# Performance work log

Hardware: AMD Instinct MI355X
Metric: run time of the kernel (lower is better)

## Reference

```python
import jax, jax.numpy as jnp
import numpy as np

DIM, NHEADS = 1536, 12
HEAD_DIM = DIM // NHEADS  # 128

def _rope_params(max_pos, d):
    inv = 1.0 / (10000.0 ** (np.arange(0, d, 2, dtype=np.float64) / d))
    ang = np.outer(np.arange(max_pos, dtype=np.float64), inv)
    return np.stack([np.cos(ang), np.sin(ang)], -1).astype(np.float32)  # [max_pos, d//2, 2]

def setup_inputs() -> dict:
    key = jax.random.key(0)
    ks = jax.random.split(key, 8)
    B, F, H, W = 1, 3, 30, 52
    L = F * H * W  # 4680
    def w(k):
        return jax.random.normal(k, (DIM, DIM), jnp.float32) * 0.02
    # Wan rope table: head_dim=128 -> segments of real dim 44, 42, 42 (complex 22,21,21)
    freqs = np.concatenate([_rope_params(1024, 44), _rope_params(1024, 42), _rope_params(1024, 42)], axis=1)
    return {
        "x": jax.random.normal(ks[0], (B, L, DIM), jnp.float32),
        "wq": w(ks[1]), "bq": jnp.zeros((DIM,), jnp.float32),
        "wk": w(ks[2]), "bk": jnp.zeros((DIM,), jnp.float32),
        "wv": w(ks[3]), "bv": jnp.zeros((DIM,), jnp.float32),
        "wo": w(ks[4]), "bo": jnp.zeros((DIM,), jnp.float32),
        "gq": jnp.ones((DIM,), jnp.float32),
        "gk": jnp.ones((DIM,), jnp.float32),
        "freqs": jnp.asarray(freqs),                       # [1024, 64, 2] (cos, sin)
        "seq_lens": jnp.array([L], jnp.int64),
        "grid_sizes": jnp.array([[F, H, W]], jnp.int64),
        "F": F, "H": H, "W": W,
        "sink_size": 1, "local_attn_size": 2,
    }

def _rmsnorm(x, g, eps=1e-6):
    xf = x.astype(jnp.float32)
    return xf * jax.lax.rsqrt(jnp.mean(xf * xf, -1, keepdims=True) + eps) * g

def _rope_table(freqs, F, H, W):
    # freqs: [1024, 64, 2]; split complex dims [22, 21, 21] for (t, h, w)
    c = freqs.shape[1]
    s0 = c - 2 * (c // 3)          # 22
    s1 = c // 3                    # 21
    ft = jnp.broadcast_to(freqs[:F, :s0].reshape(F, 1, 1, s0, 2), (F, H, W, s0, 2))
    fh = jnp.broadcast_to(freqs[:H, s0:s0 + s1].reshape(1, H, 1, s1, 2), (F, H, W, s1, 2))
    fw = jnp.broadcast_to(freqs[:W, s0 + s1:].reshape(1, 1, W, s1, 2), (F, H, W, s1, 2))
    return jnp.concatenate([ft, fh, fw], -2).reshape(F * H * W, c, 2)  # [L, c, 2]

def _apply_rope(t, fr):
    # t: [B, L, n, d]; fr: [L, c, 2] with c = d // 2; complex multiply in real arithmetic
    B, L, n, d = t.shape
    c = d // 2
    tr = t.reshape(B, L, n, c, 2)
    a, b = tr[..., 0], tr[..., 1]
    cos = fr[None, :, None, :, 0]
    sin = fr[None, :, None, :, 1]
    out = jnp.stack([a * cos - b * sin, a * sin + b * cos], -1)
    return out.reshape(B, L, n, d)

def reference(x, wq, bq, wk, bk, wv, bv, wo, bo, gq, gk, freqs, seq_lens, grid_sizes,
              F, H, W, sink_size, local_attn_size):
    B, L, dim = x.shape
    n, d = NHEADS, HEAD_DIM
    q = _rmsnorm(x @ wq.T + bq, gq).reshape(B, L, n, d)
    k = _rmsnorm(x @ wk.T + bk, gk).reshape(B, L, n, d)
    v = (x @ wv.T + bv).reshape(B, L, n, d)
    fr = _rope_table(freqs, F, H, W)
    rq = _apply_rope(q, fr)
    rk = _apply_rope(k, fr)
    # sink + causal local-window block mask at frame granularity
    frame = jnp.arange(L) // (H * W)
    fq, fk = frame[:, None], frame[None, :]
    allow = (fk <= fq) & ((fk < sink_size) | (fq - fk < local_attn_size))  # [L, L]
    scores = jnp.einsum('blnd,bmnd->bnlm', rq, rk) / jnp.sqrt(jnp.float32(d))
    scores = jnp.where(allow[None, None], scores, -jnp.inf)
    p = jax.nn.softmax(scores, axis=-1)
    out = jnp.einsum('bnlm,bmnd->blnd', p, v).reshape(B, L, dim)
    return out @ wo.T + bo
```

## Files before the change

### kernel.cpp

```cpp
#include <hip/hip_runtime.h>

#define L_SEQ 4680
#define DIMSZ 1536
#define NHEAD 12
#define HDIM 128
#define FRAME 1560
#define NKT_ALL 74
#define SCALE_L2E 0.12751743f
#define WSZ 2359296
#define XSZ 7274496
#define PMPITCH 4736

typedef float f32x4 __attribute__((ext_vector_type(4)));
typedef _Float16 f16;
typedef _Float16 f16x2 __attribute__((ext_vector_type(2)));
typedef _Float16 f16x4 __attribute__((ext_vector_type(4)));
typedef _Float16 f16x8 __attribute__((ext_vector_type(8)));
typedef unsigned short u16;

__device__ __forceinline__ void gll16(const void* g, void* l) {
  __builtin_amdgcn_global_load_lds(
      (const __attribute__((address_space(1))) unsigned int*)g,
      (__attribute__((address_space(3))) unsigned int*)l, 16, 0, 0);
}

__global__ __launch_bounds__(256) void split_a16(
    const float* __restrict__ A, int R, f16* __restrict__ out) {
  const int rt = blockIdx.x, kt = blockIdx.y;
  const int t = threadIdx.x;
  const int row = t >> 1, c0 = (t & 1) * 16;
  const int gr = min(rt * 128 + row, R - 1);
  const float* src = &A[(size_t)gr * DIMSZ + kt * 32 + c0];
  float f[16];
#pragma unroll
  for (int i = 0; i < 4; ++i) *(float4*)&f[i * 4] = *(const float4*)&src[i * 4];
  size_t obase = ((size_t)(rt * 48 + kt)) * 4096 + row * 32;
#pragma unroll
  for (int cc = 0; cc < 2; ++cc) {
    f16x8 o;
#pragma unroll
    for (int i = 0; i < 8; ++i) o[i] = (f16)f[cc * 8 + i];
    int s = (c0 >> 3) + cc;
    *(f16x8*)&out[obase + ((s * 8) ^ ((row & 3) * 8))] = o;
  }
}

__global__ __launch_bounds__(256) void split_w16(
    const float* __restrict__ A, f16* __restrict__ hi, f16* __restrict__ lo8) {
  const int rt = blockIdx.x, kt = blockIdx.y;
  const int t = threadIdx.x;
  const int row = t >> 1, c0 = (t & 1) * 16;
  const float* src = &A[(size_t)(rt * 128 + row) * DIMSZ + kt * 32 + c0];
  float f[16];
#pragma unroll
  for (int i = 0; i < 4; ++i) *(float4*)&f[i * 4] = *(const float4*)&src[i * 4];
  size_t obase = ((size_t)(rt * 48 + kt)) * 4096 + row * 32;
#pragma unroll
  for (int cc = 0; cc < 2; ++cc) {
    f16x8 oh, ol;
#pragma unroll
    for (int i = 0; i < 8; ++i) {
      float v = f[cc * 8 + i];
      f16 h = (f16)v;
      oh[i] = h;
      ol[i] = (f16)((v - (float)h) * 256.0f);
    }
    int s = (c0 >> 3) + cc;
    size_t off = obase + ((s * 8) ^ ((row & 3) * 8));
    *(f16x8*)&hi[off] = oh;
    *(f16x8*)&lo8[off] = ol;
  }
}

__global__ __launch_bounds__(256, 3) void gemm_f16(
    const f16* __restrict__ A, const f16* __restrict__ Wh, const f16* __restrict__ Wl,
    const float* __restrict__ b0, const float* __restrict__ b1, const float* __restrict__ b2,
    float* __restrict__ C, int M) {
  __shared__ f16 S[2][3][4096];
  const int t = threadIdx.x;
  const int lane = t & 63, w = t >> 6;
  const int g = lane >> 4, ln = lane & 15;
  const int wm = w >> 1, wn = w & 1;
  const int mt = blockIdx.x, nt = blockIdx.y;
  const int which = nt / 12, ntw = nt - which * 12;
  const float* bias = which == 0 ? b0 : (which == 1 ? b1 : b2);
  const f16* srcs[3] = {A + (size_t)mt * 48 * 4096,
                        Wh + ((size_t)which * 12 + ntw) * 48 * 4096,
                        Wl + ((size_t)which * 12 + ntw) * 48 * 4096};
  float* Cw = C + (size_t)which * ((size_t)L_SEQ * DIMSZ);
  f32x4 acc[4][4] = {};
#pragma unroll
  for (int a = 0; a < 3; ++a)
#pragma unroll
    for (int i = 0; i < 2; ++i)
      gll16(srcs[a] + (i * 256 + t) * 8, &S[0][a][(i * 256 + t) * 8]);
  int buf = 0;
  const f16 sc = (f16)0.00390625f;
  for (int kt = 0; kt < 48; ++kt) {
    __syncthreads();
    if (kt + 1 < 48) {
      int b = buf ^ 1;
#pragma unroll
      for (int a = 0; a < 3; ++a)
#pragma unroll
        for (int i = 0; i < 2; ++i)
          gll16(srcs[a] + (size_t)(kt + 1) * 4096 + (i * 256 + t) * 8,
                &S[b][a][(i * 256 + t) * 8]);
    }
    f16x8 af[4], as[4], wh4[4], wl4[4];
#pragma unroll
    for (int mi = 0; mi < 4; ++mi) {
      int row = wm * 64 + mi * 16 + ln;
      int off = row * 32 + ((g * 8) ^ ((row & 3) * 8));
      af[mi] = *(const f16x8*)&S[buf][0][off];
#pragma unroll
      for (int i = 0; i < 8; ++i) as[mi][i] = af[mi][i] * sc;
    }
#pragma unroll
    for (int ni = 0; ni < 4; ++ni) {
      int row = wn * 64 + ni * 16 + ln;
      int off = row * 32 + ((g * 8) ^ ((row & 3) * 8));
      wh4[ni] = *(const f16x8*)&S[buf][1][off];
      wl4[ni] = *(const f16x8*)&S[buf][2][off];
    }
#pragma unroll
    for (int mi = 0; mi < 4; ++mi)
#pragma unroll
      for (int ni = 0; ni < 4; ++ni) {
        acc[mi][ni] = __builtin_amdgcn_mfma_f32_16x16x32_f16(af[mi], wh4[ni], acc[mi][ni], 0, 0, 0);
        acc[mi][ni] = __builtin_amdgcn_mfma_f32_16x16x32_f16(as[mi], wl4[ni], acc[mi][ni], 0, 0, 0);
      }
    buf ^= 1;
  }
#pragma unroll
  for (int mi = 0; mi < 4; ++mi)
#pragma unroll
    for (int ni = 0; ni < 4; ++ni) {
      int col = ntw * 128 + wn * 64 + ni * 16 + ln;
      float bv = bias[col];
#pragma unroll
      for (int r = 0; r < 4; ++r) {
        int row = mt * 128 + wm * 64 + mi * 16 + 4 * g + r;
        if (row < M) Cw[(size_t)row * DIMSZ + col] = acc[mi][ni][r] + bv;
      }
    }
}

__global__ __launch_bounds__(256) void norm_rope(
    const float* __restrict__ qf, const float* __restrict__ kf,
    const float* __restrict__ gq, const float* __restrict__ gk,
    const float* __restrict__ freqs, f16* __restrict__ q16, f16* __restrict__ k16) {
  const int pos = blockIdx.x;
  const bool isq = blockIdx.y == 0;
  const float* row = (isq ? qf : kf) + (size_t)pos * DIMSZ;
  const float* g = isq ? gq : gk;
  const int t = threadIdx.x;
  float2 ab[3];
  float ss = 0.f;
#pragma unroll
  for (int i = 0; i < 3; ++i) {
    ab[i] = *(const float2*)&row[2 * (t + 256 * i)];
    ss += ab[i].x * ab[i].x + ab[i].y * ab[i].y;
  }
#pragma unroll
  for (int m = 32; m; m >>= 1) ss += __shfl_xor(ss, m);
  __shared__ float part[4];
  if ((t & 63) == 0) part[t >> 6] = ss;
  __syncthreads();
  const float tot = part[0] + part[1] + part[2] + part[3];
  float scale = rsqrtf(tot * (1.f / DIMSZ) + 1e-6f);
  if (isq) scale *= SCALE_L2E;
  const int f = pos / FRAME;
  const int rem = pos - f * FRAME;
  const int hh = rem / 52;
  const int ww = rem - hh * 52;
  const int kt = pos >> 6, kk = pos & 63;
#pragma unroll
  for (int i = 0; i < 3; ++i) {
    const int p = t + 256 * i;
    const int c = p & 63;
    const int h = p >> 6;
    const int pr = c < 22 ? f : (c < 43 ? hh : ww);
    const float cs = freqs[(pr * 64 + c) * 2 + 0];
    const float sn = freqs[(pr * 64 + c) * 2 + 1];
    const float a = ab[i].x * scale * g[2 * p];
    const float b = ab[i].y * scale * g[2 * p + 1];
    f16x2 o;
    o[0] = (f16)(a * cs - b * sn);
    o[1] = (f16)(a * sn + b * cs);
    if (isq) {
      *(f16x2*)&q16[(size_t)pos * DIMSZ + 2 * p] = o;
    } else {
      const int s = c >> 2;
      size_t base = ((size_t)(h * NKT_ALL + kt)) << 13;
      *(f16x2*)&k16[base + kk * 128 + ((s * 8) ^ ((kk & 7) * 8)) + (c & 3) * 2] = o;
    }
  }
}

__global__ __launch_bounds__(256) void vconvert(const float* __restrict__ v, f16* __restrict__ v16) {
  __shared__ f16 Ls[64][136];
  const int kt = blockIdx.x, h = blockIdx.y, t = threadIdx.x;
#pragma unroll
  for (int p = 0; p < 8; ++p) {
    int e = p * 1024 + t * 4;
    int kk = e >> 7, d = e & 127;
    int gr = kt * 64 + kk;
    float4 val = make_float4(0.f, 0.f, 0.f, 0.f);
    if (gr < L_SEQ) val = *(const float4*)&v[(size_t)gr * DIMSZ + h * HDIM + d];
    f16x4 o;
    o[0] = (f16)val.x; o[1] = (f16)val.y; o[2] = (f16)val.z; o[3] = (f16)val.w;
    *(f16x4*)&Ls[kk][d] = o;
  }
  __syncthreads();
  f16* out = v16 + (((size_t)(h * NKT_ALL + kt)) << 13);
#pragma unroll
  for (int p = 0; p < 4; ++p) {
    int idx = p * 256 + t;
    int d = idx >> 3, kg = idx & 7;
    f16x8 o;
#pragma unroll
    for (int i = 0; i < 8; ++i) o[i] = Ls[kg * 8 + i][d];
    *(f16x8*)&out[d * 64 + ((kg * 8) ^ ((d & 7) * 8))] = o;
  }
}

__global__ __launch_bounds__(256, 2) void attn_split(
    const f16* __restrict__ q16, const f16* __restrict__ k16,
    const f16* __restrict__ v16, float* __restrict__ pO,
    float* __restrict__ pm, float* __restrict__ pl) {
  __shared__ f16 Ks[2][8192];
  __shared__ f16 Vt[2][8192];
  __shared__ float Os[4][16][20];
  const int b = blockIdx.x;
  const int qt = 36 - b / 24;
  const int rem = b % 24;
  const int s = rem / 12;
  const int h = rem % 12;
  const int q0 = qt * 128;
  const int t = threadIdx.x;
  const int lane = t & 63, w = t >> 6;
  const int g = lane >> 4, ln = lane & 15;

  f16x8 qa[2][4];
  int klim[2];
  float m_run[2], l_run[2];
#pragma unroll
  for (int mi = 0; mi < 2; ++mi) {
    int qrow = min(q0 + w * 32 + mi * 16 + ln, L_SEQ - 1);
    klim[mi] = (qrow / FRAME + 1) * FRAME;
    m_run[mi] = -1e30f;
    l_run[mi] = 0.f;
    const f16* qb = &q16[(size_t)qrow * DIMSZ + h * HDIM + g * 8];
#pragma unroll
    for (int kc = 0; kc < 4; ++kc) qa[mi][kc] = *(const f16x8*)&qb[kc * 32];
  }
  const int klim0 = __shfl(klim[0], 0);
  f32x4 acc[2][8] = {};

  const int rmax = min(q0 + 127, L_SEQ - 1);
  const int nkt = ((rmax / FRAME + 1) * FRAME + 63) >> 6;
  const size_t hbase = ((size_t)h * NKT_ALL) << 13;
  {
    size_t tb = hbase + ((size_t)s << 13);
#pragma unroll
    for (int i = 0; i < 4; ++i) {
      gll16(k16 + tb + (i * 256 + t) * 8, &Ks[0][(i * 256 + t) * 8]);
      gll16(v16 + tb + (i * 256 + t) * 8, &Vt[0][(i * 256 + t) * 8]);
    }
  }
  int buf = 0;
  for (int kt = s; kt < nkt; kt += 2) {
    __syncthreads();
    if (kt + 2 < nkt) {
      size_t tb = hbase + ((size_t)(kt + 2) << 13);
      int nb_ = buf ^ 1;
#pragma unroll
      for (int i = 0; i < 4; ++i) {
        gll16(k16 + tb + (i * 256 + t) * 8, &Ks[nb_][(i * 256 + t) * 8]);
        gll16(v16 + tb + (i * 256 + t) * 8, &Vt[nb_][(i * 256 + t) * 8]);
      }
    }
    const f16* Kb = Ks[buf];
    const f16* Vb = Vt[buf];

    f32x4 st[2][4] = {};
    __builtin_amdgcn_s_setprio(1);
#pragma unroll
    for (int nb = 0; nb < 4; ++nb) {
      int row = nb * 16 + ln;
      f16x8 kb[4];
#pragma unroll
      for (int kc = 0; kc < 4; ++kc)
        kb[kc] = *(const f16x8*)&Kb[row * 128 + ((g * 8 + kc * 32) ^ ((row & 7) * 8))];
#pragma unroll
      for (int kc = 0; kc < 4; ++kc) {
        st[0][nb] = __builtin_amdgcn_mfma_f32_16x16x32_f16(kb[kc], qa[0][kc], st[0][nb], 0, 0, 0);
        st[1][nb] = __builtin_amdgcn_mfma_f32_16x16x32_f16(kb[kc], qa[1][kc], st[1][nb], 0, 0, 0);
      }
    }
    __builtin_amdgcn_s_setprio(0);

    f16x4 pb[2][4];
    const bool boundary = (kt * 64 + 64 > klim0);
#pragma unroll
    for (int mi = 0; mi < 2; ++mi) {
      float pv4[4][4];
      float rm = -1e30f;
      if (boundary) {
#pragma unroll
        for (int nb = 0; nb < 4; ++nb)
#pragma unroll
          for (int r = 0; r < 4; ++r) {
            int key = kt * 64 + nb * 16 + 4 * g + r;
            float val = st[mi][nb][r];
            if (key >= klim[mi]) val = -1e30f;
            pv4[nb][r] = val;
            rm = fmaxf(rm, val);
          }
      } else {
#pragma unroll
        for (int nb = 0; nb < 4; ++nb)
#pragma unroll
          for (int r = 0; r < 4; ++r) {
            float val = st[mi][nb][r];
            pv4[nb][r] = val;
            rm = fmaxf(rm, val);
          }
      }
      rm = fmaxf(rm, __shfl_xor(rm, 16));
      rm = fmaxf(rm, __shfl_xor(rm, 32));
      if (!__all(rm - m_run[mi] <= 8.0f)) {
        float mn = fmaxf(m_run[mi], rm);
        float fs = exp2f(m_run[mi] - mn);
        m_run[mi] = mn;
        l_run[mi] *= fs;
#pragma unroll
        for (int db = 0; db < 8; ++db)
#pragma unroll
          for (int r = 0; r < 4; ++r) acc[mi][db][r] *= fs;
      }
      float sm = 0.f;
#pragma unroll
      for (int nb = 0; nb < 4; ++nb)
#pragma unroll
        for (int r = 0; r < 4; ++r) {
          float e = exp2f(pv4[nb][r] - m_run[mi]);
          sm += e;
          pb[mi][nb][r] = (f16)e;
        }
      sm += __shfl_xor(sm, 16);
      sm += __shfl_xor(sm, 32);
      l_run[mi] += sm;
    }

    __builtin_amdgcn_s_setprio(1);
#pragma unroll
    for (int db = 0; db < 8; ++db) {
      int d = db * 16 + ln;
#pragma unroll
      for (int nb = 0; nb < 4; ++nb) {
        f16x4 va = *(const f16x4*)&Vb[d * 64 + ((nb * 16 + 4 * g) ^ ((d & 7) * 8))];
        acc[0][db] = __builtin_amdgcn_mfma_f32_16x16x16f16(va, pb[0][nb], acc[0][db], 0, 0, 0);
        acc[1][db] = __builtin_amdgcn_mfma_f32_16x16x16f16(va, pb[1][nb], acc[1][db], 0, 0, 0);
      }
    }
    __builtin_amdgcn_s_setprio(0);
    buf ^= 1;
  }

#pragma unroll
  for (int mi = 0; mi < 2; ++mi) {
    int qrow = q0 + w * 32 + mi * 16 + ln;
    if (g == 0) {
      pm[((size_t)s * 12 + h) * PMPITCH + qrow] = m_run[mi];
      pl[((size_t)s * 12 + h) * PMPITCH + qrow] = l_run[mi];
    }
#pragma unroll
    for (int db = 0; db < 8; ++db) {
      *(f32x4*)&Os[w][ln][4 * g] = acc[mi][db];
      asm volatile("s_waitcnt lgkmcnt(0)" ::: "memory");
#pragma unroll
      for (int r = 0; r < 4; ++r) {
        int q = q0 + w * 32 + mi * 16 + 4 * g + r;
        float val = Os[w][4 * g + r][ln];
        if (q < L_SEQ)
          pO[((size_t)s * L_SEQ + q) * DIMSZ + h * HDIM + db * 16 + ln] = val;
      }
      asm volatile("s_waitcnt lgkmcnt(0)" ::: "memory");
    }
  }
}

__global__ __launch_bounds__(256) void combine_k(
    const float* __restrict__ pO, const float* __restrict__ pm,
    const float* __restrict__ pl, f16* __restrict__ aos) {
  const int qt = blockIdx.x, h = blockIdx.y, t = threadIdx.x;
  const int row = t >> 1, d0 = (t & 1) * 64;
  const int q = min(qt * 128 + row, L_SEQ - 1);
  const float m0 = pm[(size_t)h * PMPITCH + q];
  const float m1 = pm[((size_t)12 + h) * PMPITCH + q];
  const float l0 = pl[(size_t)h * PMPITCH + q];
  const float l1 = pl[((size_t)12 + h) * PMPITCH + q];
  const float m = fmaxf(m0, m1);
  float w0 = exp2f(m0 - m), w1 = exp2f(m1 - m);
  const float rinv = 1.f / (w0 * l0 + w1 * l1);
  w0 *= rinv; w1 *= rinv;
  const float* o0 = &pO[(size_t)q * DIMSZ + h * HDIM + d0];
  const float* o1 = &pO[((size_t)L_SEQ + q) * DIMSZ + h * HDIM + d0];
  f16* outbase = aos + ((size_t)qt * 48 + h * 4) * 4096 + row * 32;
#pragma unroll
  for (int c8 = 0; c8 < 8; ++c8) {
    float a[8], bvals[8];
    *(float4*)&a[0] = *(const float4*)&o0[c8 * 8];
    *(float4*)&a[4] = *(const float4*)&o0[c8 * 8 + 4];
    *(float4*)&bvals[0] = *(const float4*)&o1[c8 * 8];
    *(float4*)&bvals[4] = *(const float4*)&o1[c8 * 8 + 4];
    f16x8 ov;
#pragma unroll
    for (int i = 0; i < 8; ++i) ov[i] = (f16)(w0 * a[i] + w1 * bvals[i]);
    int d = d0 + c8 * 8;
    int ktb = d >> 5;
    int s8 = (d & 31) >> 3;
    *(f16x8*)&outbase[(size_t)ktb * 4096 + ((s8 * 8) ^ ((row & 3) * 8))] = ov;
  }
}

extern "C" void kernel_launch(void* const* d_in, const int* in_sizes, int n_in,
                              void* d_out, int out_size, void* d_ws, size_t ws_size,
                              hipStream_t stream) {
  const float* x  = (const float*)d_in[0];
  const float* wq = (const float*)d_in[1];
  const float* bq = (const float*)d_in[2];
  const float* wk = (const float*)d_in[3];
  const float* bk = (const float*)d_in[4];
  const float* wv = (const float*)d_in[5];
  const float* bv = (const float*)d_in[6];
  const float* wo = (const float*)d_in[7];
  const float* bo = (const float*)d_in[8];
  const float* gq = (const float*)d_in[9];
  const float* gk = (const float*)d_in[10];
  const float* freqs = (const float*)d_in[11];
  float* out = (float*)d_out;
  float* ws = (float*)d_ws;

  const size_t LD = (size_t)L_SEQ * DIMSZ;

  float* qf = ws;
  float* kf = ws + LD;
  float* vf = ws + 2 * LD;
  f16* xs  = (f16*)(ws + 3 * LD);
  f16* k16 = xs + XSZ;
  f16* v16 = k16 + XSZ;
  f16* whi = v16 + XSZ;
  f16* wlo = whi + 3 * (size_t)WSZ;
  f16* q16 = xs;
  float* pO = qf;
  f16* aos = (f16*)vf;
  float* pm = vf + XSZ / 2;
  float* pl = pm + 2 * 12 * PMPITCH;
  f16* wo_hi = (f16*)(pl + 2 * 12 * PMPITCH);
  f16* wo_lo = wo_hi + (size_t)WSZ;

  dim3 blk(256);
  split_a16<<<dim3(37, 48), blk, 0, stream>>>(x, L_SEQ, xs);
  split_w16<<<dim3(12, 48), blk, 0, stream>>>(wq, whi, wlo);
  split_w16<<<dim3(12, 48), blk, 0, stream>>>(wk, whi + (size_t)WSZ, wlo + (size_t)WSZ);
  split_w16<<<dim3(12, 48), blk, 0, stream>>>(wv, whi + 2 * (size_t)WSZ, wlo + 2 * (size_t)WSZ);
  gemm_f16<<<dim3(37, 36), blk, 0, stream>>>(xs, whi, wlo, bq, bk, bv, qf, L_SEQ);
  norm_rope<<<dim3(L_SEQ, 2), blk, 0, stream>>>(qf, kf, gq, gk, freqs, q16, k16);
  vconvert<<<dim3(NKT_ALL, NHEAD), blk, 0, stream>>>(vf, v16);
  split_w16<<<dim3(12, 48), blk, 0, stream>>>(wo, wo_hi, wo_lo);
  attn_split<<<dim3(37 * 24), blk, 0, stream>>>(q16, k16, v16, pO, pm, pl);
  combine_k<<<dim3(37, 12), blk, 0, stream>>>(pO, pm, pl, aos);
  gemm_f16<<<dim3(37, 12), blk, 0, stream>>>(aos, wo_hi, wo_lo, bo, bo, bo, out, L_SEQ);
}
```

Before: 452.8 us.

## Register-staged single-buffer attention with 3 blocks/CU, wider V reads, fused weight split

The attention kernel drops its double-buffered LDS tiles, which used async global-to-LDS loads, in favour of a single LDS buffer. The next K/V tile is prefetched into registers and written to LDS after an extra barrier, which halves LDS use so launch bounds can allow 3 blocks per CU instead of 2. The V transpose layout is changed so the PV stage reads 8 halves per LDS load instead of 4. The three Q/K/V weight-split launches are merged into one 3D-grid launch. The trade-offs are more registers and an extra barrier per tile, which could limit the occupancy gain.

```diff
diff --git a/kernel.cpp b/kernel.cpp
--- a/kernel.cpp
+++ b/kernel.cpp
@@ -42,6 +42,38 @@
     for (int i = 0; i < 8; ++i) o[i] = (f16)f[cc * 8 + i];
     int s = (c0 >> 3) + cc;
     *(f16x8*)&out[obase + ((s * 8) ^ ((row & 3) * 8))] = o;
+  }
+}
+
+__global__ __launch_bounds__(256) void split_w16x3(
+    const float* __restrict__ s0, const float* __restrict__ s1, const float* __restrict__ s2,
+    f16* __restrict__ hi_base, f16* __restrict__ lo_base) {
+  const int z = blockIdx.z;
+  const float* A = z == 0 ? s0 : (z == 1 ? s1 : s2);
+  f16* hi = hi_base + (size_t)z * WSZ;
+  f16* lo8 = lo_base + (size_t)z * WSZ;
+  const int rt = blockIdx.x, kt = blockIdx.y;
+  const int t = threadIdx.x;
+  const int row = t >> 1, c0 = (t & 1) * 16;
+  const float* src = &A[(size_t)(rt * 128 + row) * DIMSZ + kt * 32 + c0];
+  float f[16];
+#pragma unroll
+  for (int i = 0; i < 4; ++i) *(float4*)&f[i * 4] = *(const float4*)&src[i * 4];
+  size_t obase = ((size_t)(rt * 48 + kt)) * 4096 + row * 32;
+#pragma unroll
+  for (int cc = 0; cc < 2; ++cc) {
+    f16x8 oh, ol;
+#pragma unroll
+    for (int i = 0; i < 8; ++i) {
+      float v = f[cc * 8 + i];
+      f16 h = (f16)v;
+      oh[i] = h;
+      ol[i] = (f16)((v - (float)h) * 256.0f);
+    }
+    int s = (c0 >> 3) + cc;
+    size_t off = obase + ((s * 8) ^ ((row & 3) * 8));
+    *(f16x8*)&hi[off] = oh;
+    *(f16x8*)&lo8[off] = ol;
   }
 }
 
@@ -217,20 +249,22 @@
 #pragma unroll
   for (int p = 0; p < 4; ++p) {
     int idx = p * 256 + t;
-    int d = idx >> 3, kg = idx & 7;
+    int d = idx >> 3, c = idx & 7;
+    const int nbb = (c & 1) * 2;
+    const int g4 = (c >> 1) * 4;
     f16x8 o;
 #pragma unroll
-    for (int i = 0; i < 8; ++i) o[i] = Ls[kg * 8 + i][d];
-    *(f16x8*)&out[d * 64 + ((kg * 8) ^ ((d & 7) * 8))] = o;
-  }
-}
-
-__global__ __launch_bounds__(256, 2) void attn_split(
+    for (int i = 0; i < 8; ++i) o[i] = Ls[(nbb + (i >> 2)) * 16 + g4 + (i & 3)][d];
+    *(f16x8*)&out[d * 64 + 8 * (c ^ (d & 7))] = o;
+  }
+}
+
+__global__ __launch_bounds__(256, 3) void attn_split(
     const f16* __restrict__ q16, const f16* __restrict__ k16,
     const f16* __restrict__ v16, float* __restrict__ pO,
     float* __restrict__ pm, float* __restrict__ pl) {
-  __shared__ f16 Ks[2][8192];
-  __shared__ f16 Vt[2][8192];
+  __shared__ f16 Ks[8192];
+  __shared__ f16 Vt[8192];
   __shared__ float Os[4][16][20];
   const int b = blockIdx.x;
   const int qt = 36 - b / 24;
@@ -261,28 +295,31 @@
   const int rmax = min(q0 + 127, L_SEQ - 1);
   const int nkt = ((rmax / FRAME + 1) * FRAME + 63) >> 6;
   const size_t hbase = ((size_t)h * NKT_ALL) << 13;
-  {
-    size_t tb = hbase + ((size_t)s << 13);
+
+  f16x8 kreg[4], vreg[4];
+  auto LOAD = [&](int kt_) {
+    size_t tb = hbase + ((size_t)kt_ << 13);
 #pragma unroll
     for (int i = 0; i < 4; ++i) {
-      gll16(k16 + tb + (i * 256 + t) * 8, &Ks[0][(i * 256 + t) * 8]);
-      gll16(v16 + tb + (i * 256 + t) * 8, &Vt[0][(i * 256 + t) * 8]);
-    }
-  }
-  int buf = 0;
-  for (int kt = s; kt < nkt; kt += 2) {
+      kreg[i] = *(const f16x8*)&k16[tb + (i * 256 + t) * 8];
+      vreg[i] = *(const f16x8*)&v16[tb + (i * 256 + t) * 8];
+    }
+  };
+  auto WRITE = [&]() {
+#pragma unroll
+    for (int i = 0; i < 4; ++i) {
+      *(f16x8*)&Ks[(i * 256 + t) * 8] = kreg[i];
+      *(f16x8*)&Vt[(i * 256 + t) * 8] = vreg[i];
+    }
+  };
+
+  LOAD(s);
+  WRITE();
+  int kt = s;
+  while (true) {
     __syncthreads();
-    if (kt + 2 < nkt) {
-      size_t tb = hbase + ((size_t)(kt + 2) << 13);
-      int nb_ = buf ^ 1;
-#pragma unroll
-      for (int i = 0; i < 4; ++i) {
-        gll16(k16 + tb + (i * 256 + t) * 8, &Ks[nb_][(i * 256 + t) * 8]);
-        gll16(v16 + tb + (i * 256 + t) * 8, &Vt[nb_][(i * 256 + t) * 8]);
-      }
-    }
-    const f16* Kb = Ks[buf];
-    const f16* Vb = Vt[buf];
+    const bool more = (kt + 2 < nkt);
+    if (more) LOAD(kt + 2);
 
     f32x4 st[2][4] = {};
     __builtin_amdgcn_s_setprio(1);
@@ -292,7 +329,7 @@
       f16x8 kb[4];
 #pragma unroll
       for (int kc = 0; kc < 4; ++kc)
-        kb[kc] = *(const f16x8*)&Kb[row * 128 + ((g * 8 + kc * 32) ^ ((row & 7) * 8))];
+        kb[kc] = *(const f16x8*)&Ks[row * 128 + ((g * 8 + kc * 32) ^ ((row & 7) * 8))];
 #pragma unroll
       for (int kc = 0; kc < 4; ++kc) {
         st[0][nb] = __builtin_amdgcn_mfma_f32_16x16x32_f16(kb[kc], qa[0][kc], st[0][nb], 0, 0, 0);
@@ -359,14 +396,22 @@
     for (int db = 0; db < 8; ++db) {
       int d = db * 16 + ln;
 #pragma unroll
-      for (int nb = 0; nb < 4; ++nb) {
-        f16x4 va = *(const f16x4*)&Vb[d * 64 + ((nb * 16 + 4 * g) ^ ((d & 7) * 8))];
-        acc[0][db] = __builtin_amdgcn_mfma_f32_16x16x16f16(va, pb[0][nb], acc[0][db], 0, 0, 0);
-        acc[1][db] = __builtin_amdgcn_mfma_f32_16x16x16f16(va, pb[1][nb], acc[1][db], 0, 0, 0);
+      for (int nbp = 0; nbp < 2; ++nbp) {
+        f16x8 vv = *(const f16x8*)&Vt[d * 64 + 8 * ((g * 2 + nbp) ^ (d & 7))];
+        f16x4 vlo = {vv[0], vv[1], vv[2], vv[3]};
+        f16x4 vhi = {vv[4], vv[5], vv[6], vv[7]};
+        acc[0][db] = __builtin_amdgcn_mfma_f32_16x16x16f16(vlo, pb[0][2 * nbp], acc[0][db], 0, 0, 0);
+        acc[1][db] = __builtin_amdgcn_mfma_f32_16x16x16f16(vlo, pb[1][2 * nbp], acc[1][db], 0, 0, 0);
+        acc[0][db] = __builtin_amdgcn_mfma_f32_16x16x16f16(vhi, pb[0][2 * nbp + 1], acc[0][db], 0, 0, 0);
+        acc[1][db] = __builtin_amdgcn_mfma_f32_16x16x16f16(vhi, pb[1][2 * nbp + 1], acc[1][db], 0, 0, 0);
       }
     }
     __builtin_amdgcn_s_setprio(0);
-    buf ^= 1;
+
+    if (!more) break;
+    __syncthreads();
+    WRITE();
+    kt += 2;
   }
 
 #pragma unroll
@@ -464,9 +509,7 @@
 
   dim3 blk(256);
   split_a16<<<dim3(37, 48), blk, 0, stream>>>(x, L_SEQ, xs);
-  split_w16<<<dim3(12, 48), blk, 0, stream>>>(wq, whi, wlo);
-  split_w16<<<dim3(12, 48), blk, 0, stream>>>(wk, whi + (size_t)WSZ, wlo + (size_t)WSZ);
-  split_w16<<<dim3(12, 48), blk, 0, stream>>>(wv, whi + 2 * (size_t)WSZ, wlo + 2 * (size_t)WSZ);
+  split_w16x3<<<dim3(12, 48, 3), blk, 0, stream>>>(wq, wk, wv, whi, wlo);
   gemm_f16<<<dim3(37, 36), blk, 0, stream>>>(xs, whi, wlo, bq, bk, bv, qf, L_SEQ);
   norm_rope<<<dim3(L_SEQ, 2), blk, 0, stream>>>(qf, kf, gq, gk, freqs, q16, k16);
   vconvert<<<dim3(NKT_ALL, NHEAD), blk, 0, stream>>>(vf, v16);
```

After: 624.7 us. 1.38x slower.
